# Kernel optimization log

Measured on AMD Instinct MI355X. Metric: run time of the kernel, lower is better.

## Reference

```python
import jax, jax.numpy as jnp
import numpy as np

H = 768
R = 24


def setup_inputs() -> dict:
    key = jax.random.key(0)
    ks = jax.random.split(key, 9)
    B, S = 4, 256
    hidden = jax.random.normal(ks[0], (B, S, H), dtype=jnp.float32)
    # ConcatHandshaking fc: Linear(2H -> H); torch weight shape (out,in)=(H,2H)
    fc_w = jax.random.normal(ks[1], (H, 2 * H), dtype=jnp.float32) * (1.0 / np.sqrt(2 * H))
    fc_b = jnp.zeros((H,), dtype=jnp.float32)
    # h2t: Linear(H -> 2)
    h2t_w = jax.random.normal(ks[2], (2, H), dtype=jnp.float32) * (1.0 / np.sqrt(H))
    h2t_b = jnp.zeros((2,), dtype=jnp.float32)
    # h2h / t2t TaggingProjector: R independent Linear(H -> 3), batched as (R,3,H)
    h2h_w = jax.random.normal(ks[3], (R, 3, H), dtype=jnp.float32) * (1.0 / np.sqrt(H))
    h2h_b = jnp.zeros((R, 3), dtype=jnp.float32)
    t2t_w = jax.random.normal(ks[4], (R, 3, H), dtype=jnp.float32) * (1.0 / np.sqrt(H))
    t2t_b = jnp.zeros((R, 3), dtype=jnp.float32)
    return {
        "hidden": hidden,
        "fc_w": fc_w, "fc_b": fc_b,
        "h2t_w": h2t_w, "h2t_b": h2t_b,
        "h2h_w": h2h_w, "h2h_b": h2h_b,
        "t2t_w": t2t_w, "t2t_b": t2t_b,
    }


def _handshaking(hidden, fc_w, fc_b):
    # hidden: (B, S, H). Pairs (i, j) with i <= j in row-major (torch loop) order.
    S = hidden.shape[1]
    idx_i, idx_j = jnp.triu_indices(S)  # each (P,), P = S(S+1)/2
    # concat([h_i, h_j]) @ W^T == h_i @ Wl^T + h_j @ Wr^T  (avoids (B,P,2H) buffer)
    Wl = fc_w[:, :H]  # (H, H)
    Wr = fc_w[:, H:]  # (H, H)
    left = jnp.einsum('bsh,oh->bso', hidden, Wl)   # (B, S, H)
    right = jnp.einsum('bsh,oh->bso', hidden, Wr)  # (B, S, H)
    hs = jnp.tanh(left[:, idx_i, :] + right[:, idx_j, :] + fc_b)  # (B, P, H)
    return hs


def reference(hidden, fc_w, fc_b, h2t_w, h2t_b, h2h_w, h2h_b, t2t_w, t2t_b):
    hs = _handshaking(hidden, fc_w, fc_b)  # (B, P, H)
    # h2t: plain Linear(H->2), logits (no softmax in original)
    h2t = jnp.einsum('bph,oh->bpo', hs, h2t_w) + h2t_b  # (B, P, 2)
    # TaggingProjector: batched per-relation Linear(H->3), then softmax over tags
    h2h = jax.nn.softmax(jnp.einsum('bph,rth->brpt', hs, h2h_w) + h2h_b[None, :, None, :], axis=-1)
    t2t = jax.nn.softmax(jnp.einsum('bph,rth->brpt', hs, t2t_w) + t2t_b[None, :, None, :], axis=-1)
    return (h2t, h2h, t2t)
```

## Files before the change

### kernel.cpp

```cpp
#include <hip/hip_runtime.h>
#include <hip/hip_bf16.h>

#define H 768
#define SEQ 256
#define NPAIR 32896
#define NOUTP 160
#define OFF_H2H 263168u
#define OFF_T2T 9737216u

#define N_BPK 122880
#define N_FCW 1179648
#define SCL 2.8853900817779268f

typedef short bf16x8 __attribute__((ext_vector_type(8)));
typedef float f32x4 __attribute__((ext_vector_type(4)));

__device__ __forceinline__ float tanh_s(float xs) {
    float e = __builtin_amdgcn_exp2f(xs);
    return fmaf(-2.0f, __builtin_amdgcn_rcpf(e + 1.0f), 1.0f);
}
__device__ __forceinline__ float bf_lo(int w){ return __uint_as_float(((unsigned)w) << 16); }
__device__ __forceinline__ float bf_hi(int w){ return __uint_as_float(((unsigned)w) & 0xffff0000u); }
__device__ __forceinline__ int cvtpk(float lo, float hi) {
    int r;
    asm("v_cvt_pk_bf16_f32 %0, %1, %2" : "=v"(r) : "v"(lo), "v"(hi));
    return r;
}
__device__ __forceinline__ unsigned short bf16r(float x){
    unsigned int u = __float_as_uint(x);
    u += 0x7fffu + ((u >> 16) & 1u);
    return (unsigned short)(u >> 16);
}
__device__ __forceinline__ bf16x8 tanh_frag(int4 lv, int4 rv) {
    int4 st;
    st.x = cvtpk(tanh_s(bf_lo(lv.x) + bf_lo(rv.x)), tanh_s(bf_hi(lv.x) + bf_hi(rv.x)));
    st.y = cvtpk(tanh_s(bf_lo(lv.y) + bf_lo(rv.y)), tanh_s(bf_hi(lv.y) + bf_hi(rv.y)));
    st.z = cvtpk(tanh_s(bf_lo(lv.z) + bf_lo(rv.z)), tanh_s(bf_hi(lv.z) + bf_hi(rv.z)));
    st.w = cvtpk(tanh_s(bf_lo(lv.w) + bf_lo(rv.w)), tanh_s(bf_hi(lv.w) + bf_hi(rv.w)));
    return __builtin_bit_cast(bf16x8, st);
}

__device__ __forceinline__ int row_start(int i) { return i * SEQ - (i * (i - 1)) / 2; }
__device__ __forceinline__ void pair_ij(int p, int& oi, int& oj) {
    double disc = 263169.0 - 8.0 * (double)p;
    int i = (int)((513.0 - sqrt(disc)) * 0.5);
    if (i > 0 && row_start(i) > p) --i;
    while (row_start(i + 1) <= p) ++i;
    oi = i;
    oj = i + (p - row_start(i));
}

__global__ __launch_bounds__(256) void pack_kernel(
    const float* __restrict__ h2t_w, const float* __restrict__ h2h_w,
    const float* __restrict__ t2t_w, const float* __restrict__ h2t_b,
    const float* __restrict__ h2h_b, const float* __restrict__ t2t_b,
    const float* __restrict__ fc_w,
    unsigned short* __restrict__ Bpk, unsigned short* __restrict__ fcwb,
    float* __restrict__ bc)
{
    int idx = blockIdx.x * 256 + threadIdx.x;
    if (idx < N_BPK) {
        int j = idx & 7, lane = (idx >> 3) & 63, rest = idx >> 9;
        int f = rest % 10, k32 = rest / 10;
        int n = f * 16 + (lane & 15);
        int k = k32 * 32 + ((lane >> 4) << 3) + j;
        float v = 0.f;
        if (n < 2)        v = h2t_w[n * H + k];
        else if (n < 74)  v = h2h_w[(n - 2) * H + k];
        else if (n < 146) v = t2t_w[(n - 74) * H + k];
        Bpk[idx] = bf16r(v);
    } else if (idx < N_BPK + N_FCW) {
        int q = idx - N_BPK;
        int n = q / H, k = q % H;
        float v = (n < H) ? fc_w[(size_t)n * 2 * H + k]
                          : fc_w[(size_t)(n - H) * 2 * H + H + k];
        fcwb[q] = bf16r(v);
    } else if (idx < N_BPK + N_FCW + NOUTP) {
        int q = idx - N_BPK - N_FCW;
        float v = 0.f;
        if (q < 2)        v = h2t_b[q];
        else if (q < 74)  v = h2h_b[q - 2];
        else if (q < 146) v = t2t_b[q - 74];
        bc[q] = v;
    }
}

__global__ __launch_bounds__(256, 2) void lr_mfma(
    const float* __restrict__ hidden, const unsigned short* __restrict__ fcwb,
    const float* __restrict__ fc_b,
    unsigned short* __restrict__ LB, unsigned short* __restrict__ RB)
{
    __shared__ __align__(16) char sm[24576];
    const int tid = threadIdx.x, l = tid & 63, w = tid >> 6;
    const int wm = w >> 1, wn = w & 1;
    const int m0 = blockIdx.x * 64, n0 = blockIdx.y * 128;
    f32x4 acc[2][4] = {};
    for (int c = 0; c < 12; ++c) {
        const int k0 = c * 64;
        #pragma unroll
        for (int it = 0; it < 2; ++it) {
            int idx = tid + it * 256;
            int row = idx >> 3, k8 = idx & 7;
            const float4* src = reinterpret_cast<const float4*>(hidden + (size_t)(m0 + row) * H + k0 + k8 * 8);
            float4 a = src[0], bq = src[1];
            int4 st;
            st.x = cvtpk(a.x, a.y);  st.y = cvtpk(a.z, a.w);
            st.z = cvtpk(bq.x, bq.y); st.w = cvtpk(bq.z, bq.w);
            *reinterpret_cast<int4*>(sm + row * 128 + ((k8 * 16) ^ ((row & 7) << 4))) = st;
        }
        #pragma unroll
        for (int it = 0; it < 4; ++it) {
            int idx = tid + it * 256;
            int row = idx >> 3, k8 = idx & 7;
            *reinterpret_cast<int4*>(sm + 8192 + row * 128 + ((k8 * 16) ^ ((row & 7) << 4))) =
                *reinterpret_cast<const int4*>(fcwb + (size_t)(n0 + row) * H + k0 + k8 * 8);
        }
        __syncthreads();
        #pragma unroll
        for (int kk = 0; kk < 2; ++kk) {
            const int sl = kk * 4 + (l >> 4);
            const int swz = (l & 7) << 4;
            bf16x8 af[2], bfr[4];
            #pragma unroll
            for (int a = 0; a < 2; ++a) {
                int row = 32 * wm + 16 * a + (l & 15);
                af[a] = *reinterpret_cast<const bf16x8*>(sm + row * 128 + ((sl * 16) ^ swz));
            }
            #pragma unroll
            for (int f = 0; f < 4; ++f) {
                int row = 64 * wn + 16 * f + (l & 15);
                bfr[f] = *reinterpret_cast<const bf16x8*>(sm + 8192 + row * 128 + ((sl * 16) ^ swz));
            }
            #pragma unroll
            for (int a = 0; a < 2; ++a)
                #pragma unroll
                for (int f = 0; f < 4; ++f)
                    acc[a][f] = __builtin_amdgcn_mfma_f32_16x16x32_bf16(af[a], bfr[f], acc[a][f], 0, 0, 0);
        }
        __syncthreads();
    }
    #pragma unroll
    for (int a = 0; a < 2; ++a)
        #pragma unroll
        for (int f = 0; f < 4; ++f)
            #pragma unroll
            for (int r = 0; r < 4; ++r) {
                int row = m0 + 32 * wm + 16 * a + 4 * (l >> 4) + r;
                int col = n0 + 64 * wn + 16 * f + (l & 15);
                float v = acc[a][f][r];
                if (n0 < H) LB[(size_t)row * H + col] = bf16r((v + fc_b[col]) * SCL);
                else        RB[(size_t)row * H + (col - H)] = bf16r(v * SCL);
            }
}

__global__ __launch_bounds__(256, 3) void pair_mfma(
    const unsigned short* __restrict__ LB, const unsigned short* __restrict__ RB,
    const unsigned short* __restrict__ Bpk, const float* __restrict__ bc,
    float* __restrict__ out)
{
    __shared__ __align__(16) char sm[42624];
    int*   iOf  = reinterpret_cast<int*>(sm + 40960);
    int*   jOf  = reinterpret_cast<int*>(sm + 41472);
    float* bc_s = reinterpret_cast<float*>(sm + 41984);

    const int tid = threadIdx.x, l = tid & 63, w = tid >> 6;
    const int b = blockIdx.y, p0 = blockIdx.x * 128;

    if (tid < 128) {
        int i, j; pair_ij(p0 + tid, i, j);
        iOf[tid] = i * H; jOf[tid] = j * H;
    }
    if (tid < NOUTP) bc_s[tid] = bc[tid];
    __syncthreads();

    const unsigned short* LBb = LB + (size_t)b * SEQ * H;
    const unsigned short* RBb = RB + (size_t)b * SEQ * H;
    const int row0 = 32 * w + (l & 15);
    const int kb = (l >> 4) << 3;
    const unsigned short* lp0 = LBb + iOf[row0] + kb;
    const unsigned short* rp0 = RBb + jOf[row0] + kb;
    const unsigned short* lp1 = LBb + iOf[row0 + 16] + kb;
    const unsigned short* rp1 = RBb + jOf[row0 + 16] + kb;

    const int4* bsrc = reinterpret_cast<const int4*>(Bpk);
    f32x4 acc[2][10] = {};

    int4 nb0 = bsrc[tid], nb1 = bsrc[tid + 256], nb2 = bsrc[tid + 512],
         nb3 = bsrc[tid + 768], nb4 = bsrc[tid + 1024];
    int4 lA0 = *reinterpret_cast<const int4*>(lp0);
    int4 lA1 = *reinterpret_cast<const int4*>(lp0 + 32);
    int4 lB0 = *reinterpret_cast<const int4*>(lp1);
    int4 lB1 = *reinterpret_cast<const int4*>(lp1 + 32);
    int4 rA0 = *reinterpret_cast<const int4*>(rp0);
    int4 rA1 = *reinterpret_cast<const int4*>(rp0 + 32);
    int4 rB0 = *reinterpret_cast<const int4*>(rp1);
    int4 rB1 = *reinterpret_cast<const int4*>(rp1 + 32);
    {
        int4* bw = reinterpret_cast<int4*>(sm);
        bw[tid] = nb0; bw[tid + 256] = nb1; bw[tid + 512] = nb2;
        bw[tid + 768] = nb3; bw[tid + 1024] = nb4;
    }
    __syncthreads();

    #pragma unroll 2
    for (int c = 0; c < 11; ++c) {
        const int4* bn = bsrc + (c + 1) * 1280;
        nb0 = bn[tid]; nb1 = bn[tid + 256]; nb2 = bn[tid + 512];
        nb3 = bn[tid + 768]; nb4 = bn[tid + 1024];
        bf16x8 a00 = tanh_frag(lA0, rA0);
        bf16x8 a10 = tanh_frag(lB0, rB0);
        bf16x8 a01 = tanh_frag(lA1, rA1);
        bf16x8 a11 = tanh_frag(lB1, rB1);
        const int co = (c + 1) * 64;
        lA0 = *reinterpret_cast<const int4*>(lp0 + co);
        lA1 = *reinterpret_cast<const int4*>(lp0 + co + 32);
        lB0 = *reinterpret_cast<const int4*>(lp1 + co);
        lB1 = *reinterpret_cast<const int4*>(lp1 + co + 32);
        rA0 = *reinterpret_cast<const int4*>(rp0 + co);
        rA1 = *reinterpret_cast<const int4*>(rp0 + co + 32);
        rB0 = *reinterpret_cast<const int4*>(rp1 + co);
        rB1 = *reinterpret_cast<const int4*>(rp1 + co + 32);
        const char* bufc = sm + ((c & 1) ? 20480 : 0);
        #pragma unroll
        for (int f = 0; f < 10; ++f) {
            bf16x8 bf0 = *reinterpret_cast<const bf16x8*>(bufc + (f * 64 + l) * 16);
            acc[0][f] = __builtin_amdgcn_mfma_f32_16x16x32_bf16(a00, bf0, acc[0][f], 0, 0, 0);
            acc[1][f] = __builtin_amdgcn_mfma_f32_16x16x32_bf16(a10, bf0, acc[1][f], 0, 0, 0);
        }
        #pragma unroll
        for (int f = 0; f < 10; ++f) {
            bf16x8 bf1 = *reinterpret_cast<const bf16x8*>(bufc + ((10 + f) * 64 + l) * 16);
            acc[0][f] = __builtin_amdgcn_mfma_f32_16x16x32_bf16(a01, bf1, acc[0][f], 0, 0, 0);
            acc[1][f] = __builtin_amdgcn_mfma_f32_16x16x32_bf16(a11, bf1, acc[1][f], 0, 0, 0);
        }
        int4* bufn = reinterpret_cast<int4*>(sm + (((c + 1) & 1) ? 20480 : 0));
        bufn[tid] = nb0; bufn[tid + 256] = nb1; bufn[tid + 512] = nb2;
        bufn[tid + 768] = nb3; bufn[tid + 1024] = nb4;
        __syncthreads();
    }
    {
        bf16x8 a00 = tanh_frag(lA0, rA0);
        bf16x8 a10 = tanh_frag(lB0, rB0);
        bf16x8 a01 = tanh_frag(lA1, rA1);
        bf16x8 a11 = tanh_frag(lB1, rB1);
        const char* bufc = sm + 20480;
        #pragma unroll
        for (int f = 0; f < 10; ++f) {
            bf16x8 bf0 = *reinterpret_cast<const bf16x8*>(bufc + (f * 64 + l) * 16);
            acc[0][f] = __builtin_amdgcn_mfma_f32_16x16x32_bf16(a00, bf0, acc[0][f], 0, 0, 0);
            acc[1][f] = __builtin_amdgcn_mfma_f32_16x16x32_bf16(a10, bf0, acc[1][f], 0, 0, 0);
        }
        #pragma unroll
        for (int f = 0; f < 10; ++f) {
            bf16x8 bf1 = *reinterpret_cast<const bf16x8*>(bufc + ((10 + f) * 64 + l) * 16);
            acc[0][f] = __builtin_amdgcn_mfma_f32_16x16x32_bf16(a01, bf1, acc[0][f], 0, 0, 0);
            acc[1][f] = __builtin_amdgcn_mfma_f32_16x16x32_bf16(a11, bf1, acc[1][f], 0, 0, 0);
        }
    }
    __syncthreads();

    float* scw = reinterpret_cast<float*>(sm);
    for (int s = 0; s < 4; ++s) {
        if (w == s) {
            #pragma unroll
            for (int m = 0; m < 2; ++m)
                #pragma unroll
                for (int f = 0; f < 10; ++f)
                    #pragma unroll
                    for (int r = 0; r < 4; ++r) {
                        int rl = 16 * m + 4 * (l >> 4) + r;
                        scw[rl * 172 + f * 16 + (l & 15)] = acc[m][f][r];
                    }
        }
        __syncthreads();
        if (tid < 64) {
            int rl = tid >> 1, tt = tid & 1;
            int p = p0 + 32 * s + rl;
            out[((size_t)b * NPAIR + p) * 2 + tt] = scw[rl * 172 + tt] + bc_s[tt];
        }
        #pragma unroll
        for (int it = 0; it < 6; ++it) {
            int item = it * 256 + tid;
            int rl = item & 31, rr = item >> 5;
            int ob = 2 + rr * 3;
            float l0 = scw[rl * 172 + ob + 0] + bc_s[ob + 0];
            float l1 = scw[rl * 172 + ob + 1] + bc_s[ob + 1];
            float l2 = scw[rl * 172 + ob + 2] + bc_s[ob + 2];
            float mx = fmaxf(l0, fmaxf(l1, l2));
            float e0 = __expf(l0 - mx), e1 = __expf(l1 - mx), e2 = __expf(l2 - mx);
            float inv = __fdividef(1.0f, e0 + e1 + e2);
            int p = p0 + 32 * s + rl;
            size_t base = (rr < 24)
                ? (size_t)OFF_H2H + ((size_t)(b * 24 + rr) * NPAIR + p) * 3
                : (size_t)OFF_T2T + ((size_t)(b * 24 + rr - 24) * NPAIR + p) * 3;
            out[base + 0] = e0 * inv;
            out[base + 1] = e1 * inv;
            out[base + 2] = e2 * inv;
        }
        __syncthreads();
    }
}

extern "C" void kernel_launch(void* const* d_in, const int* in_sizes, int n_in,
                              void* d_out, int out_size, void* d_ws, size_t ws_size,
                              hipStream_t stream) {
    const float* hidden = (const float*)d_in[0];
    const float* fc_w   = (const float*)d_in[1];
    const float* fc_b   = (const float*)d_in[2];
    const float* h2t_w  = (const float*)d_in[3];
    const float* h2t_b  = (const float*)d_in[4];
    const float* h2h_w  = (const float*)d_in[5];
    const float* h2h_b  = (const float*)d_in[6];
    const float* t2t_w  = (const float*)d_in[7];
    const float* t2t_b  = (const float*)d_in[8];

    char* wsb = (char*)d_ws;
    unsigned short* LBw  = (unsigned short*)(wsb);
    unsigned short* RBw  = (unsigned short*)(wsb + 1572864);
    unsigned short* Bpk  = (unsigned short*)(wsb + 3145728);
    unsigned short* fcwb = (unsigned short*)(wsb + 3391488);
    float*          bc   = (float*)        (wsb + 5750784);

    float* out = (float*)d_out;

    pack_kernel<<<(N_BPK + N_FCW + NOUTP + 255) / 256, 256, 0, stream>>>(
        h2t_w, h2h_w, t2t_w, h2t_b, h2h_b, t2t_b, fc_w, Bpk, fcwb, bc);
    lr_mfma<<<dim3(16, 12), 256, 0, stream>>>(hidden, fcwb, fc_b, LBw, RBw);
    pair_mfma<<<dim3(NPAIR / 128, 4), 256, 0, stream>>>(LBw, RBw, Bpk, bc, out);
}
```

Baseline: 96.47 us.

## Use direct global-to-LDS loads for B tiles and single-pass bf16 epilogue

Replaces the register-staged copy of the packed projection weights into shared memory with global_load_lds direct-to-LDS transfers, synchronised by explicit waitcnt and barriers. The epilogue now writes all four waves' accumulators at once into a bf16 slab and runs one softmax pass over all 128 pairs, instead of four serialized per-wave rounds with barriers. Outputs use nontemporal stores. This cuts VGPR pressure, barrier count and epilogue serialization, but rounding logits to bf16 before the softmax adds error, and the hand-written vmcnt counts must match the loads actually in flight.

```diff
diff --git a/kernel.cpp b/kernel.cpp
--- a/kernel.cpp
+++ b/kernel.cpp
@@ -21,6 +21,7 @@
 }
 __device__ __forceinline__ float bf_lo(int w){ return __uint_as_float(((unsigned)w) << 16); }
 __device__ __forceinline__ float bf_hi(int w){ return __uint_as_float(((unsigned)w) & 0xffff0000u); }
+__device__ __forceinline__ float bfu(unsigned short u){ return __uint_as_float(((unsigned)u) << 16); }
 __device__ __forceinline__ int cvtpk(float lo, float hi) {
     int r;
     asm("v_cvt_pk_bf16_f32 %0, %1, %2" : "=v"(r) : "v"(lo), "v"(hi));
@@ -38,6 +39,12 @@
     st.z = cvtpk(tanh_s(bf_lo(lv.z) + bf_lo(rv.z)), tanh_s(bf_hi(lv.z) + bf_hi(rv.z)));
     st.w = cvtpk(tanh_s(bf_lo(lv.w) + bf_lo(rv.w)), tanh_s(bf_hi(lv.w) + bf_hi(rv.w)));
     return __builtin_bit_cast(bf16x8, st);
+}
+
+typedef const __attribute__((address_space(1))) unsigned int* as1_u32p;
+typedef __attribute__((address_space(3))) unsigned int* as3_u32p;
+__device__ __forceinline__ void gload_lds16(const void* g, void* l) {
+    __builtin_amdgcn_global_load_lds((as1_u32p)g, (as3_u32p)l, 16, 0, 0);
 }
 
 __device__ __forceinline__ int row_start(int i) { return i * SEQ - (i * (i - 1)) / 2; }
@@ -153,15 +160,17 @@
             }
 }
 
+#define SLAB_STR 166
+
 __global__ __launch_bounds__(256, 3) void pair_mfma(
     const unsigned short* __restrict__ LB, const unsigned short* __restrict__ RB,
     const unsigned short* __restrict__ Bpk, const float* __restrict__ bc,
     float* __restrict__ out)
 {
-    __shared__ __align__(16) char sm[42624];
-    int*   iOf  = reinterpret_cast<int*>(sm + 40960);
-    int*   jOf  = reinterpret_cast<int*>(sm + 41472);
-    float* bc_s = reinterpret_cast<float*>(sm + 41984);
+    __shared__ __align__(16) char sm[43136];
+    int*   iOf  = reinterpret_cast<int*>(sm);
+    int*   jOf  = reinterpret_cast<int*>(sm + 512);
+    float* bc_s = reinterpret_cast<float*>(sm + 42496);
 
     const int tid = threadIdx.x, l = tid & 63, w = tid >> 6;
     const int b = blockIdx.y, p0 = blockIdx.x * 128;
@@ -181,12 +190,16 @@
     const unsigned short* rp0 = RBb + jOf[row0] + kb;
     const unsigned short* lp1 = LBb + iOf[row0 + 16] + kb;
     const unsigned short* rp1 = RBb + jOf[row0 + 16] + kb;
-
-    const int4* bsrc = reinterpret_cast<const int4*>(Bpk);
+    __syncthreads();
+
+    const char* bsrc = reinterpret_cast<const char*>(Bpk) + w * 5120 + l * 16;
+    const int ldst_off = w * 5120;
+
     f32x4 acc[2][10] = {};
 
-    int4 nb0 = bsrc[tid], nb1 = bsrc[tid + 256], nb2 = bsrc[tid + 512],
-         nb3 = bsrc[tid + 768], nb4 = bsrc[tid + 1024];
+    #pragma unroll
+    for (int t = 0; t < 5; ++t) gload_lds16(bsrc + t * 1024, sm + ldst_off + t * 1024);
+    __builtin_amdgcn_sched_barrier(0);
     int4 lA0 = *reinterpret_cast<const int4*>(lp0);
     int4 lA1 = *reinterpret_cast<const int4*>(lp0 + 32);
     int4 lB0 = *reinterpret_cast<const int4*>(lp1);
@@ -195,18 +208,18 @@
     int4 rA1 = *reinterpret_cast<const int4*>(rp0 + 32);
     int4 rB0 = *reinterpret_cast<const int4*>(rp1);
     int4 rB1 = *reinterpret_cast<const int4*>(rp1 + 32);
-    {
-        int4* bw = reinterpret_cast<int4*>(sm);
-        bw[tid] = nb0; bw[tid + 256] = nb1; bw[tid + 512] = nb2;
-        bw[tid + 768] = nb3; bw[tid + 1024] = nb4;
-    }
-    __syncthreads();
+    asm volatile("s_waitcnt vmcnt(8) lgkmcnt(0)" ::: "memory");
+    __builtin_amdgcn_s_barrier();
+    __builtin_amdgcn_sched_barrier(0);
 
     #pragma unroll 2
     for (int c = 0; c < 11; ++c) {
-        const int4* bn = bsrc + (c + 1) * 1280;
-        nb0 = bn[tid]; nb1 = bn[tid + 256]; nb2 = bn[tid + 512];
-        nb3 = bn[tid + 768]; nb4 = bn[tid + 1024];
+        char* bufc = sm + ((c & 1) ? 20480 : 0);
+        char* bufn = sm + (((c + 1) & 1) ? 20480 : 0);
+        const char* bn = bsrc + (c + 1) * 20480;
+        #pragma unroll
+        for (int t = 0; t < 5; ++t) gload_lds16(bn + t * 1024, bufn + ldst_off + t * 1024);
+        __builtin_amdgcn_sched_barrier(0);
         bf16x8 a00 = tanh_frag(lA0, rA0);
         bf16x8 a10 = tanh_frag(lB0, rB0);
         bf16x8 a01 = tanh_frag(lA1, rA1);
@@ -220,7 +233,6 @@
         rA1 = *reinterpret_cast<const int4*>(rp0 + co + 32);
         rB0 = *reinterpret_cast<const int4*>(rp1 + co);
         rB1 = *reinterpret_cast<const int4*>(rp1 + co + 32);
-        const char* bufc = sm + ((c & 1) ? 20480 : 0);
         #pragma unroll
         for (int f = 0; f < 10; ++f) {
             bf16x8 bf0 = *reinterpret_cast<const bf16x8*>(bufc + (f * 64 + l) * 16);
@@ -233,10 +245,9 @@
             acc[0][f] = __builtin_amdgcn_mfma_f32_16x16x32_bf16(a01, bf1, acc[0][f], 0, 0, 0);
             acc[1][f] = __builtin_amdgcn_mfma_f32_16x16x32_bf16(a11, bf1, acc[1][f], 0, 0, 0);
         }
-        int4* bufn = reinterpret_cast<int4*>(sm + (((c + 1) & 1) ? 20480 : 0));
-        bufn[tid] = nb0; bufn[tid + 256] = nb1; bufn[tid + 512] = nb2;
-        bufn[tid + 768] = nb3; bufn[tid + 1024] = nb4;
-        __syncthreads();
+        asm volatile("s_waitcnt vmcnt(8) lgkmcnt(0)" ::: "memory");
+        __builtin_amdgcn_s_barrier();
+        __builtin_amdgcn_sched_barrier(0);
     }
     {
         bf16x8 a00 = tanh_frag(lA0, rA0);
@@ -257,47 +268,44 @@
             acc[1][f] = __builtin_amdgcn_mfma_f32_16x16x32_bf16(a11, bf1, acc[1][f], 0, 0, 0);
         }
     }
+    asm volatile("s_waitcnt lgkmcnt(0)" ::: "memory");
+    __builtin_amdgcn_s_barrier();
+
+    unsigned short* slab = reinterpret_cast<unsigned short*>(sm);
+    #pragma unroll
+    for (int m = 0; m < 2; ++m)
+        #pragma unroll
+        for (int f = 0; f < 10; ++f)
+            #pragma unroll
+            for (int r = 0; r < 4; ++r) {
+                int row = 32 * w + 16 * m + 4 * (l >> 4) + r;
+                slab[row * SLAB_STR + f * 16 + (l & 15)] = bf16r(acc[m][f][r]);
+            }
     __syncthreads();
 
-    float* scw = reinterpret_cast<float*>(sm);
-    for (int s = 0; s < 4; ++s) {
-        if (w == s) {
-            #pragma unroll
-            for (int m = 0; m < 2; ++m)
-                #pragma unroll
-                for (int f = 0; f < 10; ++f)
-                    #pragma unroll
-                    for (int r = 0; r < 4; ++r) {
-                        int rl = 16 * m + 4 * (l >> 4) + r;
-                        scw[rl * 172 + f * 16 + (l & 15)] = acc[m][f][r];
-                    }
-        }
-        __syncthreads();
-        if (tid < 64) {
-            int rl = tid >> 1, tt = tid & 1;
-            int p = p0 + 32 * s + rl;
-            out[((size_t)b * NPAIR + p) * 2 + tt] = scw[rl * 172 + tt] + bc_s[tt];
-        }
-        #pragma unroll
-        for (int it = 0; it < 6; ++it) {
-            int item = it * 256 + tid;
-            int rl = item & 31, rr = item >> 5;
-            int ob = 2 + rr * 3;
-            float l0 = scw[rl * 172 + ob + 0] + bc_s[ob + 0];
-            float l1 = scw[rl * 172 + ob + 1] + bc_s[ob + 1];
-            float l2 = scw[rl * 172 + ob + 2] + bc_s[ob + 2];
-            float mx = fmaxf(l0, fmaxf(l1, l2));
-            float e0 = __expf(l0 - mx), e1 = __expf(l1 - mx), e2 = __expf(l2 - mx);
-            float inv = __fdividef(1.0f, e0 + e1 + e2);
-            int p = p0 + 32 * s + rl;
-            size_t base = (rr < 24)
-                ? (size_t)OFF_H2H + ((size_t)(b * 24 + rr) * NPAIR + p) * 3
-                : (size_t)OFF_T2T + ((size_t)(b * 24 + rr - 24) * NPAIR + p) * 3;
-            out[base + 0] = e0 * inv;
-            out[base + 1] = e1 * inv;
-            out[base + 2] = e2 * inv;
-        }
-        __syncthreads();
+    {
+        int p = tid >> 1, tt = tid & 1;
+        float val = bfu(slab[p * SLAB_STR + tt]) + bc_s[tt];
+        __builtin_nontemporal_store(val, &out[((size_t)b * NPAIR + p0 + p) * 2 + tt]);
+    }
+    #pragma unroll
+    for (int it = 0; it < 24; ++it) {
+        int item = it * 256 + tid;
+        int p = item & 127, rr = item >> 7;
+        int ob = 2 + rr * 3;
+        const unsigned short* sp = slab + p * SLAB_STR + ob;
+        float l0 = bfu(sp[0]) + bc_s[ob + 0];
+        float l1 = bfu(sp[1]) + bc_s[ob + 1];
+        float l2 = bfu(sp[2]) + bc_s[ob + 2];
+        float mx = fmaxf(l0, fmaxf(l1, l2));
+        float e0 = __expf(l0 - mx), e1 = __expf(l1 - mx), e2 = __expf(l2 - mx);
+        float inv = __fdividef(1.0f, e0 + e1 + e2);
+        size_t base = (rr < 24)
+            ? (size_t)OFF_H2H + ((size_t)(b * 24 + rr) * NPAIR + p0 + p) * 3
+            : (size_t)OFF_T2T + ((size_t)(b * 24 + rr - 24) * NPAIR + p0 + p) * 3;
+        __builtin_nontemporal_store(e0 * inv, &out[base + 0]);
+        __builtin_nontemporal_store(e1 * inv, &out[base + 1]);
+        __builtin_nontemporal_store(e2 * inv, &out[base + 2]);
     }
 }
 
```

Measured after the change: 97.71 us. No clear change (+1.3%).
